# Kernel tuning notes

Hardware: AMD Instinct MI355X
Metric: run time of the kernel (lower is better)

The kernel has to match this reference:

```python
import jax, jax.numpy as jnp
import numpy as np
from jax import lax

LEAK = 0.2
SCALE = 2.0 ** 0.5

def _make_blur_kernel(upsample_factor=1):
    k1 = jnp.array([1.0, 3.0, 3.0, 1.0], dtype=jnp.float32)
    k = k1[None, :] * k1[:, None]
    k = k / jnp.sum(k)
    return k * (upsample_factor ** 2)

def _modulate(weight, s):
    # weight [O,I,k,k], s [B,I] -> [B,O,I,k,k], demodulated
    wm = s[:, None, :, None, None] * weight[None]
    d = lax.rsqrt(jnp.sum(wm * wm, axis=(2, 3, 4)) + 1e-8)  # [B,O]
    return d[:, :, None, None, None] * wm

def _conv_transpose_sample(xi, wi):
    # xi [I,H,W], wi [O,I,k,k] (already ordered as wm[o,i]); torch conv_transpose2d(stride=2, pad=0)
    k = wi.shape[-1]
    y = lax.conv_general_dilated(xi[None], jnp.flip(wi, (-2, -1)), (1, 1),
                                 [(k - 1, k - 1), (k - 1, k - 1)], lhs_dilation=(2, 2),
                                 dimension_numbers=('NCHW', 'OIHW', 'NCHW'))
    return y[0]

def _conv_same_sample(xi, wi):
    y = lax.conv_general_dilated(xi[None], wi, (1, 1), [(1, 1), (1, 1)],
                                 dimension_numbers=('NCHW', 'OIHW', 'NCHW'))
    return y[0]

def _blur(x, kern, pad):
    # upfirdn2d with up=1, down=1, pad=(pad,pad): depthwise correlate with flipped kernel
    C = x.shape[1]
    w = jnp.tile(jnp.flip(kern, (0, 1))[None, None], (C, 1, 1, 1))
    return lax.conv_general_dilated(x, w, (1, 1), [(pad, pad), (pad, pad)],
                                    feature_group_count=C,
                                    dimension_numbers=('NCHW', 'OIHW', 'NCHW'))

def _flrelu(x, b):
    y = x + b.reshape(1, -1, 1, 1)
    return jnp.where(y >= 0, y, LEAK * y) * SCALE

def setup_inputs() -> dict:
    key = jax.random.key(0)
    ks = jax.random.split(key, 15)
    B, Cin, Cout, L, H = 8, 512, 256, 512, 64
    return {
        'x': jax.random.normal(ks[0], (B, Cin, H, H), jnp.float32),
        'w1': jax.random.normal(ks[1], (B, L), jnp.float32),
        'w2': jax.random.normal(ks[2], (B, L), jnp.float32),
        'noise1': jax.random.normal(ks[3], (B, 1, 2 * H, 2 * H), jnp.float32),
        'noise2': jax.random.normal(ks[4], (B, 1, 2 * H, 2 * H), jnp.float32),
        'weight1': jax.random.normal(ks[5], (Cout, Cin, 3, 3), jnp.float32) * 0.1,
        'aff1_w': jax.random.normal(ks[6], (Cin, L), jnp.float32) * 0.04,
        'aff1_b': jax.random.normal(ks[7], (Cin,), jnp.float32) * 0.1,
        'weight2': jax.random.normal(ks[8], (Cout, Cout, 3, 3), jnp.float32) * 0.1,
        'aff2_w': jax.random.normal(ks[9], (Cout, L), jnp.float32) * 0.04,
        'aff2_b': jax.random.normal(ks[10], (Cout,), jnp.float32) * 0.1,
        'ns1': jax.random.normal(ks[11], (1, 1, 1, 1), jnp.float32) * 0.1,
        'ns2': jax.random.normal(ks[12], (1, 1, 1, 1), jnp.float32) * 0.1,
        'b1': jax.random.normal(ks[13], (Cout,), jnp.float32) * 0.1,
        'b2': jax.random.normal(ks[14], (Cout,), jnp.float32) * 0.1,
    }

def reference(x, w1, w2, noise1, noise2, weight1, aff1_w, aff1_b,
              weight2, aff2_w, aff2_b, ns1, ns2, b1, b2):
    # conv1: modulated conv_transpose (upsample), blur, noise, fused leaky relu
    s1 = w1 @ aff1_w.T + aff1_b + 1.0          # [B, Cin]
    wm1 = _modulate(weight1, s1)               # [B, O, I, 3, 3]
    y = jax.vmap(_conv_transpose_sample)(x, wm1)  # [B, O, 129, 129]
    y = _blur(y, _make_blur_kernel(2), 1)      # [B, O, 128, 128]
    y = y + ns1 * noise1
    y = _flrelu(y, b1)
    # conv2: modulated same-padding conv, noise, fused leaky relu
    s2 = w2 @ aff2_w.T + aff2_b + 1.0
    wm2 = _modulate(weight2, s2)
    y = jax.vmap(_conv_same_sample)(y, wm2)
    y = y + ns2 * noise2
    y = _flrelu(y, b2)
    return y
```

## Files before the change

### kernel.cpp

```cpp
#include <hip/hip_runtime.h>
#include <hip/hip_bf16.h>

#define SQRT2C 1.41421356237309515f
#define LEAKF 0.2f

typedef __attribute__((ext_vector_type(4))) float f32x4;
typedef __attribute__((ext_vector_type(8))) __bf16 bf16x8;
typedef unsigned int u32x4 __attribute__((ext_vector_type(4)));

#define GLOAD16(g, l) \
  __builtin_amdgcn_global_load_lds((const __attribute__((address_space(1))) void*)(const void*)(g), \
                                   (__attribute__((address_space(3))) void*)(void*)(l), 16, 0, 0)

__device__ __forceinline__ unsigned short f2bf(float f) {
  unsigned int u = __float_as_uint(f);
  unsigned int r = (u + 0x7fffu + ((u >> 16) & 1u)) >> 16;
  return (unsigned short)r;
}
__device__ __forceinline__ float bflo(unsigned int w) { return __uint_as_float(w << 16); }
__device__ __forceinline__ float bfhi(unsigned int w) { return __uint_as_float(w & 0xffff0000u); }

constexpr float B1v(int c) { return (c < 0 || c > 3) ? 0.f : ((c == 0 || c == 3) ? 1.f : 3.f); }

__global__ void k_affine(const float* __restrict__ w, const float* __restrict__ aw,
                         const float* __restrict__ ab, float* __restrict__ s, int C) {
  int wid = (blockIdx.x * blockDim.x + threadIdx.x) >> 6;
  int lane = threadIdx.x & 63;
  int b = wid / C, i = wid % C;
  const float* wr = w + (size_t)b * 512;
  const float* ar = aw + (size_t)i * 512;
  float acc = 0.f;
  #pragma unroll
  for (int l = 0; l < 512; l += 64) acc += wr[l + lane] * ar[l + lane];
  #pragma unroll
  for (int off = 32; off; off >>= 1) acc += __shfl_down(acc, off, 64);
  if (lane == 0) s[wid] = acc + ab[i] + 1.0f;
}

__global__ void k_demod(const float* __restrict__ weight, const float* __restrict__ s,
                        float* __restrict__ d, int CIN) {
  int o = blockIdx.x & 255, b = blockIdx.x >> 8;
  int t = threadIdx.x;
  const float* wr = weight + (size_t)o * CIN * 9;
  const float* sr = s + (size_t)b * CIN;
  float acc = 0.f;
  for (int i = t; i < CIN; i += 256) {
    float sv = sr[i];
    float ws = 0.f;
    #pragma unroll
    for (int k = 0; k < 9; ++k) { float w = wr[(size_t)i * 9 + k]; ws += w * w; }
    acc += sv * sv * ws;
  }
  __shared__ float red[256];
  red[t] = acc; __syncthreads();
  for (int h = 128; h; h >>= 1) { if (t < h) red[t] += red[t + h]; __syncthreads(); }
  if (t == 0) d[blockIdx.x] = rsqrtf(red[0] + 1e-8f);
}

__global__ void k_wvert(const float* __restrict__ w1, const float* __restrict__ s1,
                        const float* __restrict__ d1, unsigned short* __restrict__ Wv) {
  int t = blockIdx.x * 256 + threadIdx.x;
  int i = t & 511, o = (t >> 9) & 255, b = t >> 17;
  float sd = s1[b * 512 + i] * d1[b * 256 + o];
  const float* wp = w1 + ((size_t)o * 512 + i) * 9;
  float wm[3][3];
  #pragma unroll
  for (int ky = 0; ky < 3; ++ky)
    #pragma unroll
    for (int kx = 0; kx < 3; ++kx) wm[ky][kx] = wp[ky * 3 + kx] * sd;
  #pragma unroll
  for (int rp = 0; rp < 2; ++rp)
    #pragma unroll
    for (int u = 0; u < 3; ++u)
      #pragma unroll
      for (int kx = 0; kx < 3; ++kx) {
        float v = 0.f;
        #pragma unroll
        for (int ky = 0; ky < 3; ++ky) v += B1v(4 - 2 * u - ky + rp) * wm[ky][kx];
        Wv[(((size_t)(b * 6 + rp * 3 + kx)) * 3 + u) * 131072 + (size_t)o * 512 + i] = f2bf(v);
      }
}

__global__ void k_weff2(const float* __restrict__ w2, const float* __restrict__ s2,
                        const float* __restrict__ d2, unsigned short* __restrict__ Wm) {
  int t = blockIdx.x * 256 + threadIdx.x;
  int i = t & 255, o = (t >> 8) & 255, b = t >> 16;
  float sd = s2[b * 256 + i] * d2[b * 256 + o];
  const float* wp = w2 + ((size_t)o * 256 + i) * 9;
  #pragma unroll
  for (int k = 0; k < 9; ++k)
    Wm[((size_t)(b * 9 + k) * 256 + o) * 256 + i] = f2bf(wp[k] * sd);
}

__global__ void k_border_y1(unsigned short* __restrict__ y1p) {
  int t = blockIdx.x * 256 + threadIdx.x;
  int l = t & 31;
  int c = (t >> 5) % 516;
  int b = (t >> 5) / 516;
  int p_, q_;
  if (c < 130)      { p_ = 0;       q_ = c; }
  else if (c < 260) { p_ = 129;     q_ = c - 130; }
  else if (c < 388) { p_ = c - 259; q_ = 0; }
  else              { p_ = c - 387; q_ = 129; }
  uint4* p = (uint4*)(y1p + (((size_t)(b * 130) + p_) * 130 + q_) * 256);
  p[l] = make_uint4(0u, 0u, 0u, 0u);
}

__global__ void k_fillv(unsigned short* __restrict__ xt) {
  int t = blockIdx.x * 256 + threadIdx.x;
  int j = t & 4095;
  int r = (t >> 12) & 1;
  int b = t >> 13;
  uint4* p = (uint4*)(xt + ((size_t)(b * 66) + (r ? 65 : 0)) * 64 * 512);
  p[j] = make_uint4(0u, 0u, 0u, 0u);
}

__global__ void k_txpose(const float* __restrict__ x, unsigned short* __restrict__ xt) {
  int bid = blockIdx.x;
  int i0 = (bid & 7) * 64;
  int x0 = ((bid >> 3) & 1) * 32;
  int y  = (bid >> 4) & 63;
  int b  = bid >> 10;
  int tx = threadIdx.x & 31, ty = threadIdx.x >> 5;
  __shared__ float tile[64][33];
  const float* xp = x + ((size_t)(b * 512 + i0) * 64 + y) * 64 + x0;
  for (int ii = ty; ii < 64; ii += 8) tile[ii][tx] = xp[(size_t)ii * 4096 + tx];
  __syncthreads();
  unsigned short* op = xt + (((size_t)(b * 66) + y + 1) * 64 + x0) * 512 + i0;
  for (int xx = ty; xx < 32; xx += 8) {
    int iL = tx * 2;
    unsigned int pk = (unsigned int)f2bf(tile[iL][xx]) | ((unsigned int)f2bf(tile[iL + 1][xx]) << 16);
    *(unsigned int*)&op[(size_t)xx * 512 + iL] = pk;
  }
}

template<int CIN, int GSH, int HP, int RHO_N, int TAPS, int PANB, int OM>
__global__ __launch_bounds__(512, 2) void k_gemm8p(
    const unsigned short* __restrict__ Xt,
    const unsigned short* __restrict__ Wt,
    const float* __restrict__ noise,
    const float* __restrict__ nsp,
    const float* __restrict__ bias,
    unsigned short* __restrict__ Yb,
    float* __restrict__ Yf)
{
  constexpr int GRID = 1 << GSH;
  constexpr int NT = (GRID * GRID) / 256;
  constexpr int NKT = TAPS * (CIN / 64);
  constexpr int NIT = NKT / 2;
  constexpr int KSH = (CIN == 512) ? 3 : 2;
  constexpr int KMASK = (CIN / 64) - 1;
  constexpr int TOT = NT * RHO_N * 8;
  extern __shared__ char smem[];

  int bid0 = blockIdx.x;
  int bid = (bid0 & 7) * (TOT / 8) + (bid0 >> 3);
  int nt = bid % NT;
  int rho = (bid / NT) % RHO_N;
  int b = bid / (NT * RHO_N);
  int pix0 = nt * 256;
  int tid = threadIdx.x, lane = tid & 63, w = tid >> 6;
  int lr = lane & 15, lq = lane >> 4;
  int wr = w >> 2, wc = w & 3;
  int lhi = lane >> 3, llo = lane & 7;
  int ksrc = ((llo ^ lhi) << 3);

  const unsigned short* Wp = Wt + ((size_t)b * PANB + rho * TAPS) * 256 * CIN;
  size_t aOff = (size_t)(w * 8 + lhi) * CIN + ksrc;
  size_t bOff = (size_t)lhi * CIN + ksrc;
  const unsigned short* XtB;
  if constexpr (OM == 3) XtB = Xt + (size_t)b * HP * 64 * CIN;
  else                   XtB = Xt + ((size_t)(b * HP + (pix0 >> 7))) * 130 * CIN;

  auto stageA = [&](int buf, int t, int u) {
    int tap = t >> KSH; size_t ke = (size_t)((t & KMASK) << 6);
    const unsigned short* s = Wp + (size_t)tap * 256 * CIN + ke + (size_t)u * 64 * CIN + aOff;
    char* d = smem + buf * 65536 + u * 8192 + w * 1024;
    GLOAD16(s, d);
    GLOAD16(s + (size_t)128 * CIN, d + 16384);
  };
  auto stageB = [&](int buf, int t, int u) {
    int tap = t >> KSH; size_t ke = (size_t)((t & KMASK) << 6);
    size_t tk;
    if constexpr (OM == 3) tk = (size_t)tap * 64 * CIN + ke;
    else                   tk = ((size_t)(tap / 3) * HP + (tap % 3)) * CIN + ke;
    int c0 = w >> 2, r0 = (w & 3) * 8;
    int rowA = c0 * 64 + u * 32 + r0;
    int rowB = rowA + 128;
    char* db = smem + buf * 65536 + 32768;
    size_t sA, sB;
    if constexpr (OM == 3) { sA = (size_t)(pix0 + rowA) * CIN; sB = (size_t)(pix0 + rowB) * CIN; }
    else { sA = ((size_t)(rowA >> 7) * 130 + (rowA & 127)) * CIN;
           sB = ((size_t)(rowB >> 7) * 130 + (rowB & 127)) * CIN; }
    GLOAD16(XtB + sA + tk + bOff, db + rowA * 128);
    GLOAD16(XtB + sB + tk + bOff, db + rowB * 128);
  };

  int ldsA = (wr * 128 + lr) * 128;
  int ldsB = 32768 + (wc * 64 + lr) * 128;
  int xk[2] = { (lq * 16) ^ ((lr & 7) << 4), (64 + lq * 16) ^ ((lr & 7) << 4) };

  f32x4 acc[8][4];
  #pragma unroll
  for (int m = 0; m < 8; ++m)
    #pragma unroll
    for (int n = 0; n < 4; ++n) acc[m][n] = (f32x4){0.f, 0.f, 0.f, 0.f};

  bf16x8 af[2][4], bv[2][4];
  auto readA = [&](const char* base, int mq) {
    #pragma unroll
    for (int kk = 0; kk < 2; ++kk)
      #pragma unroll
      for (int m = 0; m < 4; ++m)
        af[kk][m] = *(const bf16x8*)(base + ldsA + (mq * 4 + m) * 2048 + xk[kk]);
  };
  auto readB = [&](const char* base, int nq) {
    #pragma unroll
    for (int kk = 0; kk < 2; ++kk)
      #pragma unroll
      for (int n = 0; n < 2; ++n)
        bv[kk][nq * 2 + n] = *(const bf16x8*)(base + ldsB + (nq * 2 + n) * 2048 + xk[kk]);
  };
  auto mma = [&](int mq, int nq) {
    __builtin_amdgcn_s_setprio(1);
    #pragma unroll
    for (int kk = 0; kk < 2; ++kk)
      #pragma unroll
      for (int m = 0; m < 4; ++m)
        #pragma unroll
        for (int n = 0; n < 2; ++n)
          acc[mq * 4 + m][nq * 2 + n] = __builtin_amdgcn_mfma_f32_16x16x32_bf16(
              af[kk][m], bv[kk][nq * 2 + n], acc[mq * 4 + m][nq * 2 + n], 0, 0, 0);
    __builtin_amdgcn_s_setprio(0);
  };

#define PH_SYNC()  __builtin_amdgcn_s_barrier(); \
                   asm volatile("s_waitcnt lgkmcnt(0)" ::: "memory")
#define PH_END()   __builtin_amdgcn_s_barrier()

  stageA(0, 0, 0); stageB(0, 0, 0); stageA(0, 0, 1); stageB(0, 0, 1);
  stageA(1, 1, 0); stageB(1, 1, 0);
  asm volatile("s_waitcnt vmcnt(4)" ::: "memory");
  __builtin_amdgcn_s_barrier();

  const char* B0 = smem;
  const char* B1 = smem + 65536;

  #pragma unroll 1
  for (int i = 0; i < NIT; ++i) {
    int a = 2 * i;
    bool nl = (i + 1 < NIT);
    readA(B0, 0); readB(B0, 0);
    stageA(1, a + 1, 1);
    PH_SYNC(); mma(0, 0); PH_END();
    readB(B0, 1);
    stageB(1, a + 1, 1);
    PH_SYNC(); mma(0, 1); PH_END();
    readA(B0, 1);
    if (nl) stageA(0, a + 2, 0);
    PH_SYNC(); mma(1, 0); PH_END();
    if (nl) stageB(0, a + 2, 0);
    PH_SYNC(); mma(1, 1);
    if (nl) { asm volatile("s_waitcnt vmcnt(4)" ::: "memory"); }
    else    { asm volatile("s_waitcnt vmcnt(0)" ::: "memory"); }
    PH_END();
    readA(B1, 0); readB(B1, 0);
    if (nl) stageA(0, a + 2, 1);
    PH_SYNC(); mma(0, 0); PH_END();
    readB(B1, 1);
    if (nl) stageB(0, a + 2, 1);
    PH_SYNC(); mma(0, 1); PH_END();
    readA(B1, 1);
    if (nl) stageA(1, a + 3, 0);
    PH_SYNC(); mma(1, 0); PH_END();
    if (nl) stageB(1, a + 3, 0);
    PH_SYNC(); mma(1, 1);
    if (nl) { asm volatile("s_waitcnt vmcnt(4)" ::: "memory"); }
    PH_END();
  }
#undef PH_SYNC
#undef PH_END

  if constexpr (OM == 2) {
    float ns = nsp[0];
    #pragma unroll
    for (int m = 0; m < 8; ++m) {
      int o = wr * 128 + m * 16 + lq * 4;
      #pragma unroll
      for (int n = 0; n < 4; ++n) {
        int pix = pix0 + wc * 64 + n * 16 + lr;
        int p = pix >> 7, q = pix & 127;
        float nz = ns * noise[((size_t)b << 14) + (p << 7) + q];
        #pragma unroll
        for (int r = 0; r < 4; ++r) {
          float v = acc[m][n][r] + nz + bias[o + r];
          v = (v >= 0.f ? v : LEAKF * v) * SQRT2C;
          __builtin_nontemporal_store(v, &Yf[(((size_t)b * 256 + o + r) << 14) + (p << 7) + q]);
        }
      }
    }
  } else {
    int rp = rho / 3, kx = rho % 3;
    #pragma unroll
    for (int m = 0; m < 8; ++m) {
      int o = wr * 128 + m * 16 + lq * 4;
      #pragma unroll
      for (int n = 0; n < 4; ++n) {
        int pix = pix0 + wc * 64 + n * 16 + lr;
        int p2 = ((pix >> 6) << 1) + rp, gxp = pix & 63;
        ushort4 pk;
        #pragma unroll
        for (int r = 0; r < 4; ++r) ((unsigned short*)&pk)[r] = f2bf(acc[m][n][r]);
        *(ushort4*)&Yb[((((size_t)(b * 3) + kx) * 128 + p2) * 64 + gxp) * 256 + o] = pk;
      }
    }
  }
}

__global__ void k_hmix(const unsigned short* __restrict__ A, const float* __restrict__ noise,
                       const float* __restrict__ nsp, const float* __restrict__ bias,
                       unsigned short* __restrict__ y1p) {
  int bid = blockIdx.x;
  int qg = bid & 15;
  int p = (bid >> 4) & 127;
  int b = bid >> 11;
  int o0 = (threadIdx.x & 31) * 8;
  int q = qg * 8 + (threadIdx.x >> 5);
  int gq = q >> 1;
  float rqf = (float)(q & 1);
  float acc[8];
  #pragma unroll
  for (int r = 0; r < 8; ++r) acc[r] = 0.f;
  #pragma unroll
  for (int v = 0; v < 3; ++v) {
    int gxx = gq + v - 1;
    float bmask = (gxx >= 0 && gxx <= 63) ? 1.f : 0.f;
    int gxc = gxx < 0 ? 0 : (gxx > 63 ? 63 : gxx);
    #pragma unroll
    for (int kx = 0; kx < 3; ++kx) {
      float C0 = B1v(4 - 2 * v - kx);
      float C1 = B1v(5 - 2 * v - kx);
      if (C0 == 0.f && C1 == 0.f) continue;
      float coef = (C0 + (C1 - C0) * rqf) * bmask;
      u32x4 av = __builtin_nontemporal_load(
          (const u32x4*)&A[(((size_t)(b * 3 + kx) * 128 + p) * 64 + gxc) * 256 + o0]);
      acc[0] += coef * bflo(av[0]); acc[1] += coef * bfhi(av[0]);
      acc[2] += coef * bflo(av[1]); acc[3] += coef * bfhi(av[1]);
      acc[4] += coef * bflo(av[2]); acc[5] += coef * bfhi(av[2]);
      acc[6] += coef * bflo(av[3]); acc[7] += coef * bfhi(av[3]);
    }
  }
  float ns = nsp[0];
  float nz = ns * noise[((size_t)b << 14) + (p << 7) + q];
  float4 bl = *(const float4*)&bias[o0];
  float4 bh = *(const float4*)&bias[o0 + 4];
  float bb[8] = {bl.x, bl.y, bl.z, bl.w, bh.x, bh.y, bh.z, bh.w};
  unsigned short ov[8];
  #pragma unroll
  for (int r = 0; r < 8; ++r) {
    float vv = acc[r] * 0.0625f + nz + bb[r];
    vv = (vv >= 0.f ? vv : LEAKF * vv) * SQRT2C;
    ov[r] = f2bf(vv);
  }
  uint4 pk;
  pk.x = (unsigned)ov[0] | ((unsigned)ov[1] << 16);
  pk.y = (unsigned)ov[2] | ((unsigned)ov[3] << 16);
  pk.z = (unsigned)ov[4] | ((unsigned)ov[5] << 16);
  pk.w = (unsigned)ov[6] | ((unsigned)ov[7] << 16);
  *(uint4*)&y1p[(((size_t)(b * 130) + p + 1) * 130 + q + 1) * 256 + o0] = pk;
}

extern "C" void kernel_launch(void* const* d_in, const int* in_sizes, int n_in,
                              void* d_out, int out_size, void* d_ws, size_t ws_size,
                              hipStream_t stream) {
  (void)in_sizes; (void)n_in; (void)out_size; (void)ws_size;
  const float* x       = (const float*)d_in[0];
  const float* w1      = (const float*)d_in[1];
  const float* w2      = (const float*)d_in[2];
  const float* noise1  = (const float*)d_in[3];
  const float* noise2  = (const float*)d_in[4];
  const float* weight1 = (const float*)d_in[5];
  const float* aff1w   = (const float*)d_in[6];
  const float* aff1b   = (const float*)d_in[7];
  const float* weight2 = (const float*)d_in[8];
  const float* aff2w   = (const float*)d_in[9];
  const float* aff2b   = (const float*)d_in[10];
  const float* ns1     = (const float*)d_in[11];
  const float* ns2     = (const float*)d_in[12];
  const float* b1      = (const float*)d_in[13];
  const float* b2      = (const float*)d_in[14];

  char* ws = (char*)d_ws;
  float* s1 = (float*)(ws + 0);
  float* s2 = (float*)(ws + 16384);
  float* d1 = (float*)(ws + 24576);
  float* d2 = (float*)(ws + 32768);
  unsigned short* xt   = (unsigned short*)(ws + 40960);
  unsigned short* Wv   = (unsigned short*)(ws + 34643968);
  unsigned short* W2m  = (unsigned short*)(ws + 72392704);
  unsigned short* A    = (unsigned short*)(ws + 81829888);
  unsigned short* y1p  = (unsigned short*)(ws + 40960);

  (void)hipFuncSetAttribute((const void*)k_gemm8p<512, 6, 66, 6, 3, 18, 3>,
                            hipFuncAttributeMaxDynamicSharedMemorySize, 131072);
  (void)hipFuncSetAttribute((const void*)k_gemm8p<256, 7, 130, 1, 9, 9, 2>,
                            hipFuncAttributeMaxDynamicSharedMemorySize, 131072);

  k_affine<<<1024, 256, 0, stream>>>(w1, aff1w, aff1b, s1, 512);
  k_affine<<<512,  256, 0, stream>>>(w2, aff2w, aff2b, s2, 256);
  k_demod<<<2048, 256, 0, stream>>>(weight1, s1, d1, 512);
  k_demod<<<2048, 256, 0, stream>>>(weight2, s2, d2, 256);
  k_wvert<<<4096, 256, 0, stream>>>(weight1, s1, d1, Wv);
  k_weff2<<<2048, 256, 0, stream>>>(weight2, s2, d2, W2m);
  k_fillv<<<256, 256, 0, stream>>>(xt);
  k_txpose<<<8192, 256, 0, stream>>>(x, xt);

  k_gemm8p<512, 6, 66, 6, 3, 18, 3><<<768, 512, 131072, stream>>>(
      xt, Wv, nullptr, nullptr, nullptr, A, nullptr);

  k_border_y1<<<516, 256, 0, stream>>>(y1p);
  k_hmix<<<16384, 256, 0, stream>>>(A, noise1, ns1, b1, y1p);
  k_gemm8p<256, 7, 130, 1, 9, 9, 2><<<512, 512, 131072, stream>>>(
      y1p, W2m, noise2, ns2, b2, nullptr, (float*)d_out);
}
```

Baseline: 399.5 us.

## Replace vertical-blur-folded conv1 GEMM with per-tap GEMM plus separate vertical mix

Conv1 used to fold the vertical blur into the modulated weights, giving 18 weight panels with 3 taps each. It now runs a plain 9-tap pointwise GEMM (one panel per kernel tap) per sample, and a new k_vmix kernel applies the vertical upsample and blur before k_hmix. Work is processed in 4 chunks of 2 batches to keep the intermediates small, and the padded-row fill kernel is removed. The aim is to cut GEMM FLOPs (9 panels with 1 tap instead of 18 with 3) at the cost of an extra bf16 intermediate pass and more launches with smaller grids.

```diff
diff --git a/kernel.cpp b/kernel.cpp
--- a/kernel.cpp
+++ b/kernel.cpp
@@ -57,28 +57,16 @@
   if (t == 0) d[blockIdx.x] = rsqrtf(red[0] + 1e-8f);
 }
 
-__global__ void k_wvert(const float* __restrict__ w1, const float* __restrict__ s1,
-                        const float* __restrict__ d1, unsigned short* __restrict__ Wv) {
+__global__ void k_wmod(const float* __restrict__ w1, const float* __restrict__ s1,
+                       const float* __restrict__ d1, unsigned short* __restrict__ Am, int b0) {
   int t = blockIdx.x * 256 + threadIdx.x;
-  int i = t & 511, o = (t >> 9) & 255, b = t >> 17;
+  int i = t & 511, o = (t >> 9) & 255, bb = t >> 17;
+  int b = b0 + bb;
   float sd = s1[b * 512 + i] * d1[b * 256 + o];
   const float* wp = w1 + ((size_t)o * 512 + i) * 9;
-  float wm[3][3];
-  #pragma unroll
-  for (int ky = 0; ky < 3; ++ky)
-    #pragma unroll
-    for (int kx = 0; kx < 3; ++kx) wm[ky][kx] = wp[ky * 3 + kx] * sd;
-  #pragma unroll
-  for (int rp = 0; rp < 2; ++rp)
-    #pragma unroll
-    for (int u = 0; u < 3; ++u)
-      #pragma unroll
-      for (int kx = 0; kx < 3; ++kx) {
-        float v = 0.f;
-        #pragma unroll
-        for (int ky = 0; ky < 3; ++ky) v += B1v(4 - 2 * u - ky + rp) * wm[ky][kx];
-        Wv[(((size_t)(b * 6 + rp * 3 + kx)) * 3 + u) * 131072 + (size_t)o * 512 + i] = f2bf(v);
-      }
+  #pragma unroll
+  for (int k = 0; k < 9; ++k)
+    Am[((size_t)(bb * 9 + k) * 256 + o) * 512 + i] = f2bf(wp[k] * sd);
 }
 
 __global__ void k_weff2(const float* __restrict__ w2, const float* __restrict__ s2,
@@ -106,15 +94,6 @@
   p[l] = make_uint4(0u, 0u, 0u, 0u);
 }
 
-__global__ void k_fillv(unsigned short* __restrict__ xt) {
-  int t = blockIdx.x * 256 + threadIdx.x;
-  int j = t & 4095;
-  int r = (t >> 12) & 1;
-  int b = t >> 13;
-  uint4* p = (uint4*)(xt + ((size_t)(b * 66) + (r ? 65 : 0)) * 64 * 512);
-  p[j] = make_uint4(0u, 0u, 0u, 0u);
-}
-
 __global__ void k_txpose(const float* __restrict__ x, unsigned short* __restrict__ xt) {
   int bid = blockIdx.x;
   int i0 = (bid & 7) * 64;
@@ -126,7 +105,7 @@
   const float* xp = x + ((size_t)(b * 512 + i0) * 64 + y) * 64 + x0;
   for (int ii = ty; ii < 64; ii += 8) tile[ii][tx] = xp[(size_t)ii * 4096 + tx];
   __syncthreads();
-  unsigned short* op = xt + (((size_t)(b * 66) + y + 1) * 64 + x0) * 512 + i0;
+  unsigned short* op = xt + ((size_t)(b * 4096) + y * 64 + x0) * 512 + i0;
   for (int xx = ty; xx < 32; xx += 8) {
     int iL = tx * 2;
     unsigned int pk = (unsigned int)f2bf(tile[iL][xx]) | ((unsigned int)f2bf(tile[iL + 1][xx]) << 16);
@@ -150,7 +129,7 @@
   constexpr int NIT = NKT / 2;
   constexpr int KSH = (CIN == 512) ? 3 : 2;
   constexpr int KMASK = (CIN / 64) - 1;
-  constexpr int TOT = NT * RHO_N * 8;
+  constexpr int TOT = NT * RHO_N * ((OM == 0) ? 2 : 8);
   extern __shared__ char smem[];
 
   int bid0 = blockIdx.x;
@@ -169,7 +148,7 @@
   size_t aOff = (size_t)(w * 8 + lhi) * CIN + ksrc;
   size_t bOff = (size_t)lhi * CIN + ksrc;
   const unsigned short* XtB;
-  if constexpr (OM == 3) XtB = Xt + (size_t)b * HP * 64 * CIN;
+  if constexpr (OM != 2) XtB = Xt + (size_t)b * GRID * 64 * CIN;
   else                   XtB = Xt + ((size_t)(b * HP + (pix0 >> 7))) * 130 * CIN;
 
   auto stageA = [&](int buf, int t, int u) {
@@ -182,14 +161,14 @@
   auto stageB = [&](int buf, int t, int u) {
     int tap = t >> KSH; size_t ke = (size_t)((t & KMASK) << 6);
     size_t tk;
-    if constexpr (OM == 3) tk = (size_t)tap * 64 * CIN + ke;
+    if constexpr (OM != 2) tk = (size_t)tap * 64 * CIN + ke;
     else                   tk = ((size_t)(tap / 3) * HP + (tap % 3)) * CIN + ke;
     int c0 = w >> 2, r0 = (w & 3) * 8;
     int rowA = c0 * 64 + u * 32 + r0;
     int rowB = rowA + 128;
     char* db = smem + buf * 65536 + 32768;
     size_t sA, sB;
-    if constexpr (OM == 3) { sA = (size_t)(pix0 + rowA) * CIN; sB = (size_t)(pix0 + rowB) * CIN; }
+    if constexpr (OM != 2) { sA = (size_t)(pix0 + rowA) * CIN; sB = (size_t)(pix0 + rowB) * CIN; }
     else { sA = ((size_t)(rowA >> 7) * 130 + (rowA & 127)) * CIN;
            sB = ((size_t)(rowB >> 7) * 130 + (rowB & 127)) * CIN; }
     GLOAD16(XtB + sA + tk + bOff, db + rowA * 128);
@@ -300,30 +279,68 @@
       }
     }
   } else {
-    int rp = rho / 3, kx = rho % 3;
     #pragma unroll
     for (int m = 0; m < 8; ++m) {
       int o = wr * 128 + m * 16 + lq * 4;
       #pragma unroll
       for (int n = 0; n < 4; ++n) {
         int pix = pix0 + wc * 64 + n * 16 + lr;
-        int p2 = ((pix >> 6) << 1) + rp, gxp = pix & 63;
         ushort4 pk;
         #pragma unroll
         for (int r = 0; r < 4; ++r) ((unsigned short*)&pk)[r] = f2bf(acc[m][n][r]);
-        *(ushort4*)&Yb[((((size_t)(b * 3) + kx) * 128 + p2) * 64 + gxp) * 256 + o] = pk;
+        *(ushort4*)&Yb[((size_t)(b * 9 + rho) * 4096 + pix) * 256 + o] = pk;
       }
     }
   }
 }
 
-__global__ void k_hmix(const unsigned short* __restrict__ A, const float* __restrict__ noise,
+__global__ void k_vmix(const unsigned short* __restrict__ Z, unsigned short* __restrict__ At) {
+  int bid = blockIdx.x;
+  int gxg = bid & 7;
+  int p = (bid >> 3) & 127;
+  int rest = bid >> 10;
+  int kx = rest % 3, bb = rest / 3;
+  int o0 = (threadIdx.x & 31) * 8;
+  int gx = gxg * 8 + (threadIdx.x >> 5);
+  int gy = p >> 1;
+  float rpf = (float)(p & 1);
+  float acc[8];
+  #pragma unroll
+  for (int r = 0; r < 8; ++r) acc[r] = 0.f;
+  #pragma unroll
+  for (int u = 0; u < 3; ++u) {
+    int gyy = gy + u - 1;
+    float bmask = (gyy >= 0 && gyy <= 63) ? 1.f : 0.f;
+    int gyc = gyy < 0 ? 0 : (gyy > 63 ? 63 : gyy);
+    #pragma unroll
+    for (int ky = 0; ky < 3; ++ky) {
+      float C0 = B1v(4 - 2 * u - ky);
+      float C1 = B1v(5 - 2 * u - ky);
+      if (C0 == 0.f && C1 == 0.f) continue;
+      float coef = (C0 + (C1 - C0) * rpf) * bmask;
+      u32x4 zv = *(const u32x4*)&Z[(((size_t)(bb * 9 + ky * 3 + kx)) * 4096 + gyc * 64 + gx) * 256 + o0];
+      acc[0] += coef * bflo(zv[0]); acc[1] += coef * bfhi(zv[0]);
+      acc[2] += coef * bflo(zv[1]); acc[3] += coef * bfhi(zv[1]);
+      acc[4] += coef * bflo(zv[2]); acc[5] += coef * bfhi(zv[2]);
+      acc[6] += coef * bflo(zv[3]); acc[7] += coef * bfhi(zv[3]);
+    }
+  }
+  u32x4 ov;
+  ov[0] = (unsigned)f2bf(acc[0]) | ((unsigned)f2bf(acc[1]) << 16);
+  ov[1] = (unsigned)f2bf(acc[2]) | ((unsigned)f2bf(acc[3]) << 16);
+  ov[2] = (unsigned)f2bf(acc[4]) | ((unsigned)f2bf(acc[5]) << 16);
+  ov[3] = (unsigned)f2bf(acc[6]) | ((unsigned)f2bf(acc[7]) << 16);
+  *(u32x4*)&At[(((size_t)(bb * 3 + kx) * 128 + p) * 64 + gx) * 256 + o0] = ov;
+}
+
+__global__ void k_hmix(const unsigned short* __restrict__ At, const float* __restrict__ noise,
                        const float* __restrict__ nsp, const float* __restrict__ bias,
-                       unsigned short* __restrict__ y1p) {
+                       unsigned short* __restrict__ y1p, int b0) {
   int bid = blockIdx.x;
   int qg = bid & 15;
   int p = (bid >> 4) & 127;
-  int b = bid >> 11;
+  int bb = bid >> 11;
+  int b = b0 + bb;
   int o0 = (threadIdx.x & 31) * 8;
   int q = qg * 8 + (threadIdx.x >> 5);
   int gq = q >> 1;
@@ -342,8 +359,7 @@
       float C1 = B1v(5 - 2 * v - kx);
       if (C0 == 0.f && C1 == 0.f) continue;
       float coef = (C0 + (C1 - C0) * rqf) * bmask;
-      u32x4 av = __builtin_nontemporal_load(
-          (const u32x4*)&A[(((size_t)(b * 3 + kx) * 128 + p) * 64 + gxc) * 256 + o0]);
+      u32x4 av = *(const u32x4*)&At[(((size_t)(bb * 3 + kx) * 128 + p) * 64 + gxc) * 256 + o0];
       acc[0] += coef * bflo(av[0]); acc[1] += coef * bfhi(av[0]);
       acc[2] += coef * bflo(av[1]); acc[3] += coef * bfhi(av[1]);
       acc[4] += coef * bflo(av[2]); acc[5] += coef * bfhi(av[2]);
@@ -354,11 +370,11 @@
   float nz = ns * noise[((size_t)b << 14) + (p << 7) + q];
   float4 bl = *(const float4*)&bias[o0];
   float4 bh = *(const float4*)&bias[o0 + 4];
-  float bb[8] = {bl.x, bl.y, bl.z, bl.w, bh.x, bh.y, bh.z, bh.w};
+  float bb8[8] = {bl.x, bl.y, bl.z, bl.w, bh.x, bh.y, bh.z, bh.w};
   unsigned short ov[8];
   #pragma unroll
   for (int r = 0; r < 8; ++r) {
-    float vv = acc[r] * 0.0625f + nz + bb[r];
+    float vv = acc[r] * 0.0625f + nz + bb8[r];
     vv = (vv >= 0.f ? vv : LEAKF * vv) * SQRT2C;
     ov[r] = f2bf(vv);
   }
@@ -396,12 +412,13 @@
   float* d1 = (float*)(ws + 24576);
   float* d2 = (float*)(ws + 32768);
   unsigned short* xt   = (unsigned short*)(ws + 40960);
-  unsigned short* Wv   = (unsigned short*)(ws + 34643968);
-  unsigned short* W2m  = (unsigned short*)(ws + 72392704);
-  unsigned short* A    = (unsigned short*)(ws + 81829888);
-  unsigned short* y1p  = (unsigned short*)(ws + 40960);
-
-  (void)hipFuncSetAttribute((const void*)k_gemm8p<512, 6, 66, 6, 3, 18, 3>,
+  unsigned short* W2m  = (unsigned short*)(ws + 33595392);
+  unsigned short* y1p  = (unsigned short*)(ws + 43032576);
+  unsigned short* Am2  = (unsigned short*)(ws + 112254976);
+  unsigned short* Z2   = (unsigned short*)(ws + 116973568);
+  unsigned short* At2  = (unsigned short*)(ws + 154722304);
+
+  (void)hipFuncSetAttribute((const void*)k_gemm8p<512, 6, 64, 9, 1, 9, 0>,
                             hipFuncAttributeMaxDynamicSharedMemorySize, 131072);
   (void)hipFuncSetAttribute((const void*)k_gemm8p<256, 7, 130, 1, 9, 9, 2>,
                             hipFuncAttributeMaxDynamicSharedMemorySize, 131072);
@@ -410,16 +427,19 @@
   k_affine<<<512,  256, 0, stream>>>(w2, aff2w, aff2b, s2, 256);
   k_demod<<<2048, 256, 0, stream>>>(weight1, s1, d1, 512);
   k_demod<<<2048, 256, 0, stream>>>(weight2, s2, d2, 256);
-  k_wvert<<<4096, 256, 0, stream>>>(weight1, s1, d1, Wv);
   k_weff2<<<2048, 256, 0, stream>>>(weight2, s2, d2, W2m);
-  k_fillv<<<256, 256, 0, stream>>>(xt);
   k_txpose<<<8192, 256, 0, stream>>>(x, xt);
-
-  k_gemm8p<512, 6, 66, 6, 3, 18, 3><<<768, 512, 131072, stream>>>(
-      xt, Wv, nullptr, nullptr, nullptr, A, nullptr);
-
   k_border_y1<<<516, 256, 0, stream>>>(y1p);
-  k_hmix<<<16384, 256, 0, stream>>>(A, noise1, ns1, b1, y1p);
+
+  for (int s = 0; s < 4; ++s) {
+    int b0 = s * 2;
+    k_wmod<<<1024, 256, 0, stream>>>(weight1, s1, d1, Am2, b0);
+    k_gemm8p<512, 6, 64, 9, 1, 9, 0><<<288, 512, 131072, stream>>>(
+        xt + (size_t)b0 * 4096 * 512, Am2, nullptr, nullptr, nullptr, Z2, nullptr);
+    k_vmix<<<6144, 256, 0, stream>>>(Z2, At2);
+    k_hmix<<<4096, 256, 0, stream>>>(At2, noise1, ns1, b1, y1p, b0);
+  }
+
   k_gemm8p<256, 7, 130, 1, 9, 9, 2><<<512, 512, 131072, stream>>>(
       y1p, W2m, noise2, ns2, b2, nullptr, (float*)d_out);
 }
```

Measured after the change: 473.0 us. 1.18x slower.
